# Kernel tuning notes

Hardware: AMD Instinct MI355X
Metric: run time of the kernel (lower is better)

## Reference

```python
import jax, jax.numpy as jnp
import numpy as np

NUM_HEADS = 16
EPS = 1e-12  # matches torch F.normalize eps


def _l2_normalize(x):
    n = jnp.sqrt(jnp.sum(x * x, axis=-1, keepdims=True))
    return x / jnp.maximum(n, EPS)


def setup_inputs() -> dict:
    key = jax.random.key(0)
    ks = jax.random.split(key, 9)
    B, L, S, D = 4, 4096, 4096, 1024
    s = 1.0 / np.sqrt(D)
    return {
        "q": jax.random.normal(ks[0], (B, L, D), jnp.float32),
        "k": jax.random.normal(ks[1], (B, S, D), jnp.float32),
        "v": jax.random.normal(ks[2], (B, S, D), jnp.float32),
        "Wq": jax.random.normal(ks[3], (D, D), jnp.float32) * s,
        "bq": jax.random.normal(ks[4], (D,), jnp.float32) * 0.01,
        "Wk": jax.random.normal(ks[5], (D, D), jnp.float32) * s,
        "bk": jax.random.normal(ks[6], (D,), jnp.float32) * 0.01,
        "Wv": jax.random.normal(ks[7], (D, D), jnp.float32) * s,
        "bv": jax.random.normal(ks[8], (D,), jnp.float32) * 0.01,
    }


def reference(q, k, v, Wq, bq, Wk, bk, Wv, bv):
    B = q.shape[0]
    H = NUM_HEADS
    # Linear projections (torch Linear: x @ W^T + b)
    qp = q @ Wq.T + bq  # [B, L, D]
    kp = k @ Wk.T + bk  # [B, S, D]
    vp = v @ Wv.T + bv  # [B, S, D]
    # Split heads: [B, T, H, i] -> [B, H, T, i]
    def split(x):
        Bx, T, D = x.shape
        return x.reshape(Bx, T, H, D // H).transpose(0, 2, 1, 3)
    qh = split(qp)
    kh = _l2_normalize(split(kp))
    vh = _l2_normalize(split(vp))
    # No softmax -> exact reassociation: (q k^T) v == q (k^T v)
    kv = jnp.einsum('bhsi,bhsj->bhij', kh, vh)  # [B, H, i, i]
    xh = jnp.einsum('bhli,bhij->bhlj', qh, kv)  # [B, H, L, i]
    # Merge heads: [B, H, L, i] -> [B, L, H*i]
    Bx, Hh, L, I = xh.shape
    return xh.transpose(0, 2, 1, 3).reshape(Bx, L, Hh * I)
```

## Files before the change

kernel.cpp:

```cpp
#include <hip/hip_runtime.h>
#include <hip/hip_bf16.h>
#include <stdint.h>

typedef __attribute__((ext_vector_type(8))) short bf16x8;
typedef __attribute__((ext_vector_type(4))) float f32x4;
typedef __attribute__((ext_vector_type(8))) unsigned short ushort8;

__device__ __forceinline__ float bf2f(unsigned short u) {
  union { unsigned int i; float f; } x; x.i = ((unsigned int)u) << 16; return x.f;
}
__device__ __forceinline__ unsigned short f2bf(float f) {
  union { __hip_bfloat16 h; unsigned short u; } x; x.h = __float2bfloat16(f); return x.u;
}

__device__ __forceinline__ void gload_lds16(const void* g, void* l) {
  __builtin_amdgcn_global_load_lds((__attribute__((address_space(1))) const void*)g,
                                   (__attribute__((address_space(3))) void*)l, 16, 0, 0);
}

__global__ __launch_bounds__(256) void cvt_kernel(const float* __restrict__ in,
                                                  unsigned short* __restrict__ out,
                                                  int n8) {
  int i = blockIdx.x * 256 + threadIdx.x;
  if (i >= n8) return;
  const float4* p = (const float4*)(in + (size_t)i * 8);
  float4 a = p[0], b = p[1];
  ushort8 o;
  o[0] = f2bf(a.x); o[1] = f2bf(a.y); o[2] = f2bf(a.z); o[3] = f2bf(a.w);
  o[4] = f2bf(b.x); o[5] = f2bf(b.y); o[6] = f2bf(b.z); o[7] = f2bf(b.w);
  *(ushort8*)(out + (size_t)i * 8) = o;
}

__global__ __launch_bounds__(256) void cvt2_kernel(const float* __restrict__ a,
                                                   const float* __restrict__ b,
                                                   unsigned short* __restrict__ oa,
                                                   unsigned short* __restrict__ ob,
                                                   int n8) {
  const float* in = blockIdx.y ? b : a;
  unsigned short* out = blockIdx.y ? ob : oa;
  int i = blockIdx.x * 256 + threadIdx.x;
  if (i >= n8) return;
  const float4* p = (const float4*)(in + (size_t)i * 8);
  float4 x = p[0], y = p[1];
  ushort8 o;
  o[0] = f2bf(x.x); o[1] = f2bf(x.y); o[2] = f2bf(x.z); o[3] = f2bf(x.w);
  o[4] = f2bf(y.x); o[5] = f2bf(y.y); o[6] = f2bf(y.z); o[7] = f2bf(y.w);
  *(ushort8*)(out + (size_t)i * 8) = o;
}

__global__ __launch_bounds__(256) void cvt3w_kernel(const float* __restrict__ a,
                                                    const float* __restrict__ b,
                                                    const float* __restrict__ c,
                                                    unsigned short* __restrict__ oa,
                                                    unsigned short* __restrict__ ob,
                                                    unsigned short* __restrict__ oc,
                                                    int n8) {
  const float* in = blockIdx.y == 0 ? a : blockIdx.y == 1 ? b : c;
  unsigned short* out = blockIdx.y == 0 ? oa : blockIdx.y == 1 ? ob : oc;
  int i = blockIdx.x * 256 + threadIdx.x;
  if (i >= n8) return;
  const float4* p = (const float4*)(in + (size_t)i * 8);
  float4 x = p[0], y = p[1];
  ushort8 o;
  o[0] = f2bf(x.x); o[1] = f2bf(x.y); o[2] = f2bf(x.z); o[3] = f2bf(x.w);
  o[4] = f2bf(y.x); o[5] = f2bf(y.y); o[6] = f2bf(y.z); o[7] = f2bf(y.w);
  *(ushort8*)(out + (size_t)i * 8) = o;
}

template <bool NORM>
__device__ __forceinline__ void gemm256_body(
    const unsigned short* __restrict__ A,
    const unsigned short* __restrict__ B,
    const float* __restrict__ bias,
    void* __restrict__ C,
    int bm, int bn,
    unsigned short (*Ab)[256][32], unsigned short (*Bb)[256][32]) {
  const int tid = threadIdx.x;
  const int widx = tid >> 6;
  const int lane = tid & 63;
  const int wr = widx >> 2;
  const int wc = widx & 3;
  const int fr = lane & 15, fkg = lane >> 4;
  const int g4 = fkg * 4;
  const int pgo = (fkg ^ ((fr >> 1) & 3)) * 8;
  const int gsrc = ((lane & 3) ^ ((lane >> 3) & 3)) * 8;
  const int srow = lane >> 2;

  f32x4 acc[8][4];
#pragma unroll
  for (int m = 0; m < 8; ++m)
#pragma unroll
    for (int n = 0; n < 4; ++n) acc[m][n] = (f32x4){0.f, 0.f, 0.f, 0.f};

  const size_t abase = (size_t)(bm * 256) * 1024;
  const size_t bbase = (size_t)(bn * 256) * 1024;

#define STG256(kt, bi)                                                          \
  {                                                                             \
    _Pragma("unroll") for (int j = 0; j < 2; ++j) {                             \
      const int r0 = widx * 32 + j * 16;                                        \
      gload_lds16(A + abase + (size_t)(r0 + srow) * 1024 + (kt) * 32 + gsrc,    \
                  &Ab[bi][r0][0]);                                              \
      gload_lds16(B + bbase + (size_t)(r0 + srow) * 1024 + (kt) * 32 + gsrc,    \
                  &Bb[bi][r0][0]);                                              \
    }                                                                           \
  }

  STG256(0, 0);
  STG256(1, 1);
  asm volatile("s_waitcnt vmcnt(4)" ::: "memory");
  __builtin_amdgcn_s_barrier();
  __builtin_amdgcn_sched_barrier(0);

  for (int kt = 0; kt < 32; ++kt) {
    const int bi = kt % 3;
    if (kt + 2 < 32) { STG256(kt + 2, (kt + 2) % 3); }

    bf16x8 af[8], bfv[4];
#pragma unroll
    for (int m = 0; m < 8; ++m)
      af[m] = *(const bf16x8*)&Ab[bi][wr * 128 + m * 16 + fr][pgo];
#pragma unroll
    for (int n = 0; n < 4; ++n)
      bfv[n] = *(const bf16x8*)&Bb[bi][wc * 64 + n * 16 + fr][pgo];

    __builtin_amdgcn_s_setprio(1);
#pragma unroll
    for (int m = 0; m < 8; ++m)
#pragma unroll
      for (int n = 0; n < 4; ++n)
        acc[m][n] = __builtin_amdgcn_mfma_f32_16x16x32_bf16(af[m], bfv[n], acc[m][n], 0, 0, 0);
    __builtin_amdgcn_s_setprio(0);

    if (kt + 2 < 32) {
      asm volatile("s_waitcnt vmcnt(4)" ::: "memory");
    } else {
      asm volatile("s_waitcnt vmcnt(0)" ::: "memory");
    }
    __builtin_amdgcn_s_barrier();
    __builtin_amdgcn_sched_barrier(0);
  }
#undef STG256

  if (NORM) {
    float bsv[4];
#pragma unroll
    for (int n = 0; n < 4; ++n) bsv[n] = bias[bn * 256 + wc * 64 + n * 16 + fr];
#pragma unroll
    for (int m = 0; m < 8; ++m) {
      float val[4][4];
      float inv[4];
#pragma unroll
      for (int j = 0; j < 4; ++j) {
        float s = 0.f;
#pragma unroll
        for (int n = 0; n < 4; ++n) {
          val[n][j] = acc[m][n][j] + bsv[n];
          s += val[n][j] * val[n][j];
        }
        s += __shfl_xor(s, 1); s += __shfl_xor(s, 2);
        s += __shfl_xor(s, 4); s += __shfl_xor(s, 8);
        inv[j] = 1.f / fmaxf(sqrtf(s), 1e-12f);
      }
#pragma unroll
      for (int n = 0; n < 4; ++n) {
        const int col = bn * 256 + wc * 64 + n * 16 + fr;
#pragma unroll
        for (int j = 0; j < 4; ++j) {
          const int row = bm * 256 + wr * 128 + m * 16 + g4 + j;
          ((unsigned short*)C)[(size_t)row * 1024 + col] = f2bf(val[n][j] * inv[j]);
        }
      }
    }
  } else {
#pragma unroll
    for (int n = 0; n < 4; ++n) {
      const int col = bn * 256 + wc * 64 + n * 16 + fr;
      const float bsv = bias[col];
#pragma unroll
      for (int m = 0; m < 8; ++m) {
#pragma unroll
        for (int j = 0; j < 4; ++j) {
          const int row = bm * 256 + wr * 128 + m * 16 + g4 + j;
          ((float*)C)[(size_t)row * 1024 + col] = acc[m][n][j] + bsv;
        }
      }
    }
  }
}

__global__ __launch_bounds__(512) void proj_norm_kernel(
    const unsigned short* __restrict__ A0, const unsigned short* __restrict__ A1,
    const unsigned short* __restrict__ B0, const unsigned short* __restrict__ B1,
    const float* __restrict__ bias0, const float* __restrict__ bias1,
    unsigned short* __restrict__ C0, unsigned short* __restrict__ C1) {
  __shared__ unsigned short Ab[3][256][32];
  __shared__ unsigned short Bb[3][256][32];
  const int flat = (blockIdx.z * 64 + blockIdx.y) * 4 + blockIdx.x;
  const int swz = (flat & 7) * 64 + (flat >> 3);
  const int zz = swz >> 8;
  const int rem = swz & 255;
  const int bm = rem >> 2, bn = rem & 3;
  gemm256_body<true>(zz ? A1 : A0, zz ? B1 : B0, zz ? bias1 : bias0,
                     zz ? (void*)C1 : (void*)C0, bm, bn, Ab, Bb);
}

__global__ __launch_bounds__(512) void final_gemm_kernel(
    const unsigned short* __restrict__ A,
    const unsigned short* __restrict__ Beff,
    const float* __restrict__ beff,
    float* __restrict__ out) {
  __shared__ unsigned short Ab[3][256][32];
  __shared__ unsigned short Bb[3][256][32];
  const int flat = blockIdx.y * 4 + blockIdx.x;
  const int swz = (flat & 7) * 32 + (flat >> 3);
  const int bm = swz >> 2, bn = swz & 3;
  const int b = bm >> 4;
  gemm256_body<false>(A, Beff + (size_t)b * 1048576, beff + b * 1024, out, bm, bn, Ab, Bb);
}

__global__ __launch_bounds__(256) void kv_part_kernel(const unsigned short* __restrict__ kh,
                                                      const unsigned short* __restrict__ vh,
                                                      float* __restrict__ kvp) {
  const int chunk = blockIdx.x, h = blockIdx.y, b = blockIdx.z;
  __shared__ unsigned short khT[64][264];
  __shared__ unsigned short vhT[64][264];
  const int tid = threadIdx.x, wid = tid >> 6, lane = tid & 63;
  const int fr = lane & 15, fk = (lane >> 4) * 8, g4 = (lane >> 4) * 4;

  const int jb = tid & 7, sb = tid >> 3;
  const size_t base = ((size_t)b * 4096 + chunk * 256) * 1024 + h * 64;
  {
    ushort8 rk[8], rv[8];
#pragma unroll
    for (int u = 0; u < 8; ++u) {
      rk[u] = *(const ushort8*)(kh + base + (size_t)(sb * 8 + u) * 1024 + jb * 8);
      rv[u] = *(const ushort8*)(vh + base + (size_t)(sb * 8 + u) * 1024 + jb * 8);
    }
#pragma unroll
    for (int jj = 0; jj < 8; ++jj) {
      ushort8 ck, cv;
#pragma unroll
      for (int u = 0; u < 8; ++u) { ck[u] = rk[u][jj]; cv[u] = rv[u][jj]; }
      *(ushort8*)&khT[jb * 8 + jj][sb * 8] = ck;
      *(ushort8*)&vhT[jb * 8 + jj][sb * 8] = cv;
    }
  }
  __syncthreads();

  f32x4 acc2[4];
#pragma unroll
  for (int n = 0; n < 4; ++n) acc2[n] = (f32x4){0.f, 0.f, 0.f, 0.f};
#pragma unroll
  for (int ks = 0; ks < 8; ++ks) {
    bf16x8 a2 = *(const bf16x8*)&khT[wid * 16 + fr][ks * 32 + fk];
    bf16x8 b2[4];
#pragma unroll
    for (int jt = 0; jt < 4; ++jt) b2[jt] = *(const bf16x8*)&vhT[jt * 16 + fr][ks * 32 + fk];
#pragma unroll
    for (int jt = 0; jt < 4; ++jt)
      acc2[jt] = __builtin_amdgcn_mfma_f32_16x16x32_bf16(a2, b2[jt], acc2[jt], 0, 0, 0);
  }
  float* dst = kvp + ((size_t)chunk * 64 + b * 16 + h) * 4096;
#pragma unroll
  for (int jt = 0; jt < 4; ++jt)
#pragma unroll
    for (int jj = 0; jj < 4; ++jj)
      dst[(wid * 16 + g4 + jj) * 64 + jt * 16 + fr] = acc2[jt][jj];
}

__global__ __launch_bounds__(256) void weff_kernel(
    const unsigned short* __restrict__ Wq,
    const float* __restrict__ bq,
    const float* __restrict__ kvp,
    unsigned short* __restrict__ Beff,
    float* __restrict__ beff) {
  const int dt = blockIdx.x, h = blockIdx.y, b = blockIdx.z;
  __shared__ float kvS[64 * 64];
  __shared__ float WqF[64 * 128];
  const int tid = threadIdx.x;

  const float* kvsrc = kvp + (size_t)(b * 16 + h) * 4096;
  for (int e = tid; e < 4096; e += 256) {
    float s = 0.f;
#pragma unroll
    for (int c = 0; c < 16; ++c) s += kvsrc[(size_t)c * 64 * 4096 + e];
    kvS[e] = s;
  }
  {
    int i = tid >> 2, dseg = tid & 3;
    const unsigned short* src = Wq + (size_t)(h * 64 + i) * 1024 + dt * 128 + dseg * 32;
    float* dst = &WqF[i * 128 + dseg * 32];
#pragma unroll
    for (int w = 0; w < 4; ++w) {
      ushort8 vv = ((const ushort8*)src)[w];
#pragma unroll
      for (int u = 0; u < 8; ++u) dst[w * 8 + u] = bf2f(vv[u]);
    }
  }
  __syncthreads();

  const int tj = tid & 63, tg = tid >> 6;
  float o[32];
#pragma unroll
  for (int dd = 0; dd < 32; ++dd) o[dd] = 0.f;
  for (int i = 0; i < 64; ++i) {
    float kvv = kvS[i * 64 + tj];
    const float* wr = &WqF[i * 128 + tg * 32];
#pragma unroll
    for (int dd = 0; dd < 32; ++dd) o[dd] += wr[dd] * kvv;
  }
  unsigned short* dstB = Beff + ((size_t)(b * 1024 + h * 64 + tj)) * 1024 + dt * 128 + tg * 32;
#pragma unroll
  for (int w = 0; w < 4; ++w) {
    ushort8 ov;
#pragma unroll
    for (int u = 0; u < 8; ++u) ov[u] = f2bf(o[w * 8 + u]);
    ((ushort8*)dstB)[w] = ov;
  }
  if (tg == 0 && dt == 0) {
    float s = 0.f;
    for (int i = 0; i < 64; ++i) s += bq[h * 64 + i] * kvS[i * 64 + tj];
    beff[b * 1024 + h * 64 + tj] = s;
  }
}

extern "C" void kernel_launch(void* const* d_in, const int* in_sizes, int n_in,
                              void* d_out, int out_size, void* d_ws, size_t ws_size,
                              hipStream_t stream) {
  const float* q = (const float*)d_in[0];
  const float* k = (const float*)d_in[1];
  const float* v = (const float*)d_in[2];
  const float* Wq = (const float*)d_in[3];
  const float* bq = (const float*)d_in[4];
  const float* Wk = (const float*)d_in[5];
  const float* bk = (const float*)d_in[6];
  const float* Wv = (const float*)d_in[7];
  const float* bv = (const float*)d_in[8];
  float* out = (float*)d_out;

  const size_t NE = (size_t)16384 * 1024;
  const size_t MB = 1048576;

  char* ws = (char*)d_ws;
  unsigned short* S0 = (unsigned short*)(ws + 0 * MB);
  unsigned short* S1 = (unsigned short*)(ws + 32 * MB);
  unsigned short* kh = (unsigned short*)(ws + 64 * MB);
  unsigned short* vh = (unsigned short*)(ws + 96 * MB);
  unsigned short* Wqb = (unsigned short*)(ws + 128 * MB);
  unsigned short* Wkb = (unsigned short*)(ws + 130 * MB);
  unsigned short* Wvb = (unsigned short*)(ws + 132 * MB);
  float* beff = (float*)(ws + 134 * MB);
  float* kvp = (float*)S0;
  unsigned short* Beff = (unsigned short*)(ws + 16 * MB);

  cvt2_kernel<<<dim3(8192, 2), 256, 0, stream>>>(k, v, S0, S1, (int)(NE / 8));
  cvt3w_kernel<<<dim3(512, 3), 256, 0, stream>>>(Wq, Wk, Wv, Wqb, Wkb, Wvb, 131072);

  proj_norm_kernel<<<dim3(4, 64, 2), 512, 0, stream>>>(S0, S1, Wkb, Wvb, bk, bv, kh, vh);

  cvt_kernel<<<8192, 256, 0, stream>>>(q, S1, (int)(NE / 8));

  kv_part_kernel<<<dim3(16, 16, 4), 256, 0, stream>>>(kh, vh, kvp);

  weff_kernel<<<dim3(8, 16, 4), 256, 0, stream>>>(Wqb, bq, kvp, Beff, beff);

  final_gemm_kernel<<<dim3(4, 64), 512, 0, stream>>>(S1, Beff, beff, out);
}
```

Baseline: 253.0 us.

## Restructure GEMM main loop into ping-pong pipeline with finer-grained staging

Replaces the 3-stage K-loop (one 32-wide K tile per iteration, one barrier per step) with a double-buffered 64-wide K pipeline. Each half is split into two B sub-quadrants, and global->LDS loads for upcoming tiles are interleaved between MFMA bursts under explicit barriers and vmcnt waits. The LDS swizzle is changed to a simpler XOR pattern, LDS buffers grow from 3 to 4 slots, and launch bounds are pinned to one block per CU. The aim is better overlap of memory traffic with MFMA work and fewer LDS bank conflicts, at the cost of many more barriers and more LDS use.

```diff
diff --git a/kernel.cpp b/kernel.cpp
--- a/kernel.cpp
+++ b/kernel.cpp
@@ -74,73 +74,99 @@
     const float* __restrict__ bias,
     void* __restrict__ C,
     int bm, int bn,
-    unsigned short (*Ab)[256][32], unsigned short (*Bb)[256][32]) {
+    unsigned short (*As)[256][32],
+    unsigned short (*Bs)[256][32]) {
   const int tid = threadIdx.x;
-  const int widx = tid >> 6;
-  const int lane = tid & 63;
-  const int wr = widx >> 2;
-  const int wc = widx & 3;
+  const int widx = tid >> 6, lane = tid & 63;
+  const int wr = widx >> 2, wc = widx & 3;
   const int fr = lane & 15, fkg = lane >> 4;
   const int g4 = fkg * 4;
-  const int pgo = (fkg ^ ((fr >> 1) & 3)) * 8;
-  const int gsrc = ((lane & 3) ^ ((lane >> 3) & 3)) * 8;
+  const int pgo = (fkg ^ (fr & 3)) * 8;
   const int srow = lane >> 2;
-
-  f32x4 acc[8][4];
-#pragma unroll
-  for (int m = 0; m < 8; ++m)
-#pragma unroll
-    for (int n = 0; n < 4; ++n) acc[m][n] = (f32x4){0.f, 0.f, 0.f, 0.f};
+  const int sg = ((lane & 3) ^ (srow & 3)) * 8;
 
   const size_t abase = (size_t)(bm * 256) * 1024;
   const size_t bbase = (size_t)(bn * 256) * 1024;
 
-#define STG256(kt, bi)                                                          \
-  {                                                                             \
-    _Pragma("unroll") for (int j = 0; j < 2; ++j) {                             \
-      const int r0 = widx * 32 + j * 16;                                        \
-      gload_lds16(A + abase + (size_t)(r0 + srow) * 1024 + (kt) * 32 + gsrc,    \
-                  &Ab[bi][r0][0]);                                              \
-      gload_lds16(B + bbase + (size_t)(r0 + srow) * 1024 + (kt) * 32 + gsrc,    \
-                  &Bb[bi][r0][0]);                                              \
-    }                                                                           \
-  }
-
-  STG256(0, 0);
-  STG256(1, 1);
-  asm volatile("s_waitcnt vmcnt(4)" ::: "memory");
-  __builtin_amdgcn_s_barrier();
-  __builtin_amdgcn_sched_barrier(0);
-
-  for (int kt = 0; kt < 32; ++kt) {
-    const int bi = kt % 3;
-    if (kt + 2 < 32) { STG256(kt + 2, (kt + 2) % 3); }
-
-    bf16x8 af[8], bfv[4];
-#pragma unroll
-    for (int m = 0; m < 8; ++m)
-      af[m] = *(const bf16x8*)&Ab[bi][wr * 128 + m * 16 + fr][pgo];
-#pragma unroll
-    for (int n = 0; n < 4; ++n)
-      bfv[n] = *(const bf16x8*)&Bb[bi][wc * 64 + n * 16 + fr][pgo];
-
-    __builtin_amdgcn_s_setprio(1);
-#pragma unroll
-    for (int m = 0; m < 8; ++m)
-#pragma unroll
-      for (int n = 0; n < 4; ++n)
-        acc[m][n] = __builtin_amdgcn_mfma_f32_16x16x32_bf16(af[m], bfv[n], acc[m][n], 0, 0, 0);
-    __builtin_amdgcn_s_setprio(0);
-
-    if (kt + 2 < 32) {
-      asm volatile("s_waitcnt vmcnt(4)" ::: "memory");
-    } else {
-      asm volatile("s_waitcnt vmcnt(0)" ::: "memory");
-    }
-    __builtin_amdgcn_s_barrier();
-    __builtin_amdgcn_sched_barrier(0);
-  }
-#undef STG256
+  f32x4 acc[8][4];
+#pragma unroll
+  for (int m = 0; m < 8; ++m)
+#pragma unroll
+    for (int n = 0; n < 4; ++n) acc[m][n] = (f32x4){0.f, 0.f, 0.f, 0.f};
+
+  bf16x8 aF[8], bF0, bF1;
+
+#define STG_A(bufi, kh, kt)                                                                \
+  {                                                                                        \
+    gload_lds16(A + abase + (size_t)(widx * 16 + srow) * 1024 + (kt) * 64 + (kh) * 32 + sg,\
+                &As[(bufi) * 2 + (kh)][widx * 16][0]);                                     \
+    gload_lds16(A + abase + (size_t)(128 + widx * 16 + srow) * 1024 + (kt) * 64 + (kh) * 32 + sg, \
+                &As[(bufi) * 2 + (kh)][128 + widx * 16][0]);                               \
+  }
+#define STG_B(bufi, kh, kt)                                                                \
+  {                                                                                        \
+    gload_lds16(B + bbase + (size_t)(widx * 16 + srow) * 1024 + (kt) * 64 + (kh) * 32 + sg,\
+                &Bs[(bufi) * 2 + (kh)][widx * 16][0]);                                     \
+    gload_lds16(B + bbase + (size_t)(128 + widx * 16 + srow) * 1024 + (kt) * 64 + (kh) * 32 + sg, \
+                &Bs[(bufi) * 2 + (kh)][128 + widx * 16][0]);                               \
+  }
+#define LDA(bufi, ks)                                                                      \
+  _Pragma("unroll") for (int m = 0; m < 8; ++m)                                            \
+      aF[m] = *(const bf16x8*)&As[(bufi) * 2 + (ks)][wr * 128 + m * 16 + fr][pgo];
+#define LDB(bufi, ks, qn)                                                                  \
+  bF0 = *(const bf16x8*)&Bs[(bufi) * 2 + (ks)][wc * 64 + (qn) * 32 + fr][pgo];             \
+  bF1 = *(const bf16x8*)&Bs[(bufi) * 2 + (ks)][wc * 64 + (qn) * 32 + 16 + fr][pgo];
+#define MM(qn)                                                                             \
+  {                                                                                        \
+    __builtin_amdgcn_s_setprio(1);                                                         \
+    _Pragma("unroll") for (int m = 0; m < 8; ++m) {                                        \
+      acc[m][(qn) * 2 + 0] =                                                               \
+          __builtin_amdgcn_mfma_f32_16x16x32_bf16(aF[m], bF0, acc[m][(qn) * 2 + 0], 0, 0, 0); \
+      acc[m][(qn) * 2 + 1] =                                                               \
+          __builtin_amdgcn_mfma_f32_16x16x32_bf16(aF[m], bF1, acc[m][(qn) * 2 + 1], 0, 0, 0); \
+    }                                                                                      \
+    __builtin_amdgcn_s_setprio(0);                                                         \
+  }
+#define BARM() asm volatile("s_barrier" ::: "memory")
+#define VMW(N) asm volatile("s_waitcnt vmcnt(" #N ")" ::: "memory")
+
+  STG_A(0, 0, 0); STG_B(0, 0, 0);
+  STG_A(0, 1, 0); STG_B(0, 1, 0);
+  STG_A(1, 0, 1); STG_B(1, 0, 1);
+  VMW(8);
+  BARM();
+
+  for (int i = 0; i < 8; ++i) {
+    const int t1s = 2 * i + 1, u0 = 2 * i + 2, u1 = 2 * i + 3;
+    const bool st = (i < 7);
+    LDA(0, 0); LDB(0, 0, 0); STG_A(1, 1, t1s);
+    BARM(); MM(0); BARM();
+    LDB(0, 0, 1); STG_B(1, 1, t1s);
+    BARM(); MM(1); VMW(8); BARM();
+    LDA(0, 1); LDB(0, 1, 0); if (st) STG_A(0, 0, u0);
+    BARM(); MM(0); BARM();
+    LDB(0, 1, 1); if (st) STG_B(0, 0, u0);
+    BARM(); MM(1);
+    if (st) { VMW(8); } else { VMW(4); }
+    BARM();
+    LDA(1, 0); LDB(1, 0, 0); if (st) STG_A(0, 1, u0);
+    BARM(); MM(0); BARM();
+    LDB(1, 0, 1); if (st) STG_B(0, 1, u0);
+    BARM(); MM(1);
+    if (st) { VMW(8); } else { VMW(0); }
+    BARM();
+    LDA(1, 1); LDB(1, 1, 0); if (st) STG_A(1, 0, u1);
+    BARM(); MM(0); BARM();
+    LDB(1, 1, 1); if (st) STG_B(1, 0, u1);
+    BARM(); MM(1); VMW(8); BARM();
+  }
+#undef STG_A
+#undef STG_B
+#undef LDA
+#undef LDB
+#undef MM
+#undef BARM
+#undef VMW
 
   if (NORM) {
     float bsv[4];
@@ -189,34 +215,34 @@
   }
 }
 
-__global__ __launch_bounds__(512) void proj_norm_kernel(
+__global__ __launch_bounds__(512, 1) void proj_norm_kernel(
     const unsigned short* __restrict__ A0, const unsigned short* __restrict__ A1,
     const unsigned short* __restrict__ B0, const unsigned short* __restrict__ B1,
     const float* __restrict__ bias0, const float* __restrict__ bias1,
     unsigned short* __restrict__ C0, unsigned short* __restrict__ C1) {
-  __shared__ unsigned short Ab[3][256][32];
-  __shared__ unsigned short Bb[3][256][32];
+  __shared__ unsigned short As[4][256][32];
+  __shared__ unsigned short Bs[4][256][32];
   const int flat = (blockIdx.z * 64 + blockIdx.y) * 4 + blockIdx.x;
   const int swz = (flat & 7) * 64 + (flat >> 3);
   const int zz = swz >> 8;
   const int rem = swz & 255;
   const int bm = rem >> 2, bn = rem & 3;
   gemm256_body<true>(zz ? A1 : A0, zz ? B1 : B0, zz ? bias1 : bias0,
-                     zz ? (void*)C1 : (void*)C0, bm, bn, Ab, Bb);
-}
-
-__global__ __launch_bounds__(512) void final_gemm_kernel(
+                     zz ? (void*)C1 : (void*)C0, bm, bn, As, Bs);
+}
+
+__global__ __launch_bounds__(512, 1) void final_gemm_kernel(
     const unsigned short* __restrict__ A,
     const unsigned short* __restrict__ Beff,
     const float* __restrict__ beff,
     float* __restrict__ out) {
-  __shared__ unsigned short Ab[3][256][32];
-  __shared__ unsigned short Bb[3][256][32];
+  __shared__ unsigned short As[4][256][32];
+  __shared__ unsigned short Bs[4][256][32];
   const int flat = blockIdx.y * 4 + blockIdx.x;
   const int swz = (flat & 7) * 32 + (flat >> 3);
   const int bm = swz >> 2, bn = swz & 3;
   const int b = bm >> 4;
-  gemm256_body<false>(A, Beff + (size_t)b * 1048576, beff + b * 1024, out, bm, bn, Ab, Bb);
+  gemm256_body<false>(A, Beff + (size_t)b * 1048576, beff + b * 1024, out, bm, bn, As, Bs);
 }
 
 __global__ __launch_bounds__(256) void kv_part_kernel(const unsigned short* __restrict__ kh,
```

After: 238.7 us. -5.7%, faster.
